# Optimization experiments

Hardware: AMD Instinct MI355X
Metric: run time of the kernel (lower is better)

## Reference

```python
import jax, jax.numpy as jnp
import numpy as np

H = 2048   # hidden_size
NH = 32    # n_head
HS = 64    # head_size
B, T = 2, 4096
D_DECAY, D_AAA, D_MV, D_GATE = 96, 96, 64, 256


def setup_inputs() -> dict:
    key = jax.random.key(0)
    ks = jax.random.split(key, 30)
    rn = lambda k, s, sc=0.02: jax.random.normal(k, s, jnp.float32) * sc
    d = {}
    d['x'] = jax.random.normal(ks[0], (B, T, H), jnp.float32)
    d['shift_state_in'] = jax.random.normal(ks[1], (B, H), jnp.float32)
    d['wkv_state_in'] = jnp.zeros((B, NH, HS, HS), jnp.float32)
    d['v_first_val'] = jax.random.normal(ks[2], (B, T, H), jnp.float32)
    for i, n in enumerate(['x_r', 'x_w', 'x_k', 'x_v', 'x_a', 'x_g']):
        d[n] = jax.random.uniform(ks[3 + i], (H,), jnp.float32)
    d['w0'] = rn(ks[9], (H,)) - 4.0
    d['w1'] = rn(ks[10], (H, D_DECAY)); d['w2'] = rn(ks[11], (D_DECAY, H))
    d['a0'] = rn(ks[12], (H,)); d['a1'] = rn(ks[13], (H, D_AAA)); d['a2'] = rn(ks[14], (D_AAA, H))
    d['v0'] = rn(ks[15], (H,)) + 1.0; d['v1'] = rn(ks[16], (H, D_MV)); d['v2'] = rn(ks[17], (D_MV, H))
    d['g1'] = rn(ks[18], (H, D_GATE)); d['g2'] = rn(ks[19], (D_GATE, H))
    d['k_k'] = jnp.full((H,), 0.85, jnp.float32)
    d['k_a'] = jnp.ones((H,), jnp.float32)
    d['r_k'] = rn(ks[20], (NH, HS))
    s = 1.0 / np.sqrt(H)
    d['W_r'] = jax.random.normal(ks[21], (H, H), jnp.float32) * s
    d['W_k'] = jax.random.normal(ks[22], (H, H), jnp.float32) * s
    d['W_v'] = jax.random.normal(ks[23], (H, H), jnp.float32) * s
    d['W_o'] = jax.random.normal(ks[24], (H, H), jnp.float32) * s
    d['ln_w'] = jnp.ones((H,), jnp.float32)
    d['ln_b'] = jnp.zeros((H,), jnp.float32)
    return d


def _forward(x, shift_state_in, wkv_state_in, v_first_val, x_r, x_w, x_k, x_v, x_a, x_g,
             w0, w1, w2, a0, a1, a2, v0, v1, v2, g1, g2, k_k, k_a, r_k,
             W_r, W_k, W_v, W_o, ln_w, ln_b):
    Bx, Tx, C = x.shape
    # token shift: previous token embedding (shift_state for t=0)
    xprev = jnp.concatenate([shift_state_in[:, None, :], x[:, :-1]], axis=1)
    dx = xprev - x
    xr, xw, xk, xv, xa, xg = (x + dx * m for m in (x_r, x_w, x_k, x_v, x_a, x_g))
    r = xr @ W_r.T
    k = xk @ W_k.T
    v = xv @ W_v.T
    # soft-clamped log-decay (<= -0.5)
    w_raw = -jax.nn.softplus(-(w0 + jnp.tanh(xw @ w1) @ w2)) - 0.5
    # layer_id > 0: residual mix with first-layer value
    v = v + (v_first_val - v) * jax.nn.sigmoid(v0 + (xv @ v1) @ v2)
    a = jax.nn.sigmoid(a0 + (xa @ a1) @ a2)          # in-context learning rate
    g = jax.nn.sigmoid(xg @ g1) @ g2                 # output gate
    kk = (k * k_k).reshape(Bx, Tx, NH, HS)
    kk = kk / jnp.maximum(jnp.linalg.norm(kk, axis=-1, keepdims=True), 1e-12)  # F.normalize
    kk = kk.reshape(Bx, Tx, C)
    k = k * (1.0 + (a - 1.0) * k_a)
    w = jnp.exp(-jnp.exp(w_raw))                     # per-channel decay in (0,1)
    heads = lambda t: t.reshape(Bx, Tx, NH, HS).transpose(1, 0, 2, 3)  # [T,B,NH,HS]
    rs, ws, ks_, vs, kks, as_ = map(heads, (r, w, k, v, kk, a))

    def step(S, inp):
        # S: [B,NH,HS(value),HS(key)]
        rt, wt, kt, vt, kkt, at = inp
        sa = jnp.einsum('bhvk,bhk->bhv', S, -kkt)
        S = (S * wt[:, :, None, :]
             + sa[:, :, :, None] * (kkt * at)[:, :, None, :]
             + vt[:, :, :, None] * kt[:, :, None, :])
        return S, jnp.einsum('bhvk,bhk->bhv', S, rt)

    wkv_state_out, y = jax.lax.scan(step, wkv_state_in, (rs, ws, ks_, vs, kks, as_))
    y = y.transpose(1, 0, 2, 3)                      # [B,T,NH,HS]
    # GroupNorm(n_head groups, eps=1e-5*head_size)
    mu = y.mean(-1, keepdims=True)
    var = y.var(-1, keepdims=True)
    y = ((y - mu) / jnp.sqrt(var + 1e-5 * HS)).reshape(Bx, Tx, C) * ln_w + ln_b
    rk = (r.reshape(Bx, Tx, NH, HS) * k.reshape(Bx, Tx, NH, HS) * r_k).sum(-1, keepdims=True)
    y = y + (rk * v.reshape(Bx, Tx, NH, HS)).reshape(Bx, Tx, C)
    out = (y * g) @ W_o.T
    return out, x[:, -1], wkv_state_out, v_first_val


def reference(x, shift_state_in, wkv_state_in, v_first_val, x_r, x_w, x_k, x_v, x_a, x_g,
              w0, w1, w2, a0, a1, a2, v0, v1, v2, g1, g2, k_k, k_a, r_k,
              W_r, W_k, W_v, W_o, ln_w, ln_b):
    return _forward(x, shift_state_in, wkv_state_in, v_first_val, x_r, x_w, x_k, x_v, x_a, x_g,
                    w0, w1, w2, a0, a1, a2, v0, v1, v2, g1, g2, k_k, k_a, r_k,
                    W_r, W_k, W_v, W_o, ln_w, ln_b)
```

## Files before the change

kernel.cpp:

```cpp
#include <hip/hip_runtime.h>

typedef unsigned short u16;
typedef __attribute__((ext_vector_type(4))) float f32x4;
typedef __attribute__((ext_vector_type(8))) __bf16 bf16x8;
typedef __attribute__((ext_vector_type(8))) unsigned short u16x8;
typedef __attribute__((ext_vector_type(4))) unsigned short u16x4;

#define DI static __device__ __forceinline__

DI float bfu2f(u16 u){ unsigned int x = ((unsigned int)u)<<16; float f; __builtin_memcpy(&f,&x,4); return f; }
DI u16 f2bfu(float f){ __bf16 h = (__bf16)f; u16 u; __builtin_memcpy(&u,&h,2); return u; }
DI float sigm(float x){ return 1.f/(1.f+expf(-x)); }

DI void gload_lds16(const void* g, void* l) {
  __builtin_amdgcn_global_load_lds(
      (const __attribute__((address_space(1))) unsigned int*)g,
      (__attribute__((address_space(3))) unsigned int*)l, 16, 0, 0);
}

template<bool OBF16>
__global__ __launch_bounds__(256) void gemm128_k(
    const u16* __restrict__ A, const u16* __restrict__ Bt,
    void* __restrict__ Cp, int M, int N, int K)
{
  __shared__ alignas(16) u16 As[128*64];
  __shared__ alignas(16) u16 Bs[128*64];
  const int tid = threadIdx.x;
  const int wid = tid >> 6, lane = tid & 63;
  const int wm = wid >> 1, wn = wid & 1;
  const int l15 = lane & 15, q = lane >> 4;
  const int m0 = blockIdx.x * 128, n0 = blockIdx.y * 128;
  const int sr = (wid << 3) + (lane >> 3);
  const int sc = (lane & 7) << 3;
  f32x4 acc[4][4];
  #pragma unroll
  for (int i=0;i<4;i++)
    #pragma unroll
    for (int j=0;j<4;j++) acc[i][j] = f32x4{0.f,0.f,0.f,0.f};

  char* la = (char*)As + (size_t)wid*1024;
  char* lb = (char*)Bs + (size_t)wid*1024;
  for (int k0 = 0; k0 < K; k0 += 64) {
    const u16* ga = A  + (size_t)(m0 + sr)*K + k0 + sc;
    const u16* gb = Bt + (size_t)(n0 + sr)*K + k0 + sc;
    #pragma unroll
    for (int it = 0; it < 4; ++it) {
      gload_lds16(ga + (size_t)(32*it)*K, la + it*4096);
      gload_lds16(gb + (size_t)(32*it)*K, lb + it*4096);
    }
    __syncthreads();
    #pragma unroll
    for (int ks = 0; ks < 64; ks += 32) {
      bf16x8 af[4], bfv[4];
      #pragma unroll
      for (int i=0;i<4;i++) af[i]  = *(const bf16x8*)&As[(wm*64 + i*16 + l15)*64 + ks + q*8];
      #pragma unroll
      for (int j=0;j<4;j++) bfv[j] = *(const bf16x8*)&Bs[(wn*64 + j*16 + l15)*64 + ks + q*8];
      #pragma unroll
      for (int i=0;i<4;i++)
        #pragma unroll
        for (int j=0;j<4;j++)
          acc[i][j] = __builtin_amdgcn_mfma_f32_16x16x32_bf16(af[i], bfv[j], acc[i][j], 0, 0, 0);
    }
    __syncthreads();
  }
  #pragma unroll
  for (int i=0;i<4;i++)
    #pragma unroll
    for (int j=0;j<4;j++)
      #pragma unroll
      for (int rr=0;rr<4;rr++) {
        const int gm = m0 + wm*64 + i*16 + q*4 + rr;
        const int gn = n0 + wn*64 + j*16 + l15;
        const size_t o = (size_t)gm * (size_t)N + gn;
        if constexpr (OBF16) ((u16*)Cp)[o] = f2bfu(acc[i][j][rr]);
        else                 ((float*)Cp)[o] = acc[i][j][rr];
      }
}

constexpr int LDW = 72;

template<bool MIX, bool WNK, bool ABF16, bool OBF16, int EPI=0>
__global__ __launch_bounds__(256) void gemm_k(
    const void* __restrict__ Ap, const float* __restrict__ dxp, const float* __restrict__ mixp,
    const float* __restrict__ Wp, void* __restrict__ Cp, int M, int N, int K)
{
  __shared__ alignas(16) __bf16 As[64*LDW];
  __shared__ alignas(16) __bf16 Bs[64*LDW];
  const int tid = threadIdx.x;
  const int m0 = blockIdx.x * 64;
  const int n0 = blockIdx.y * 64;
  const int lane = tid & 63, wid = tid >> 6;
  const int wm = wid >> 1, wn = wid & 1;
  const int l15 = lane & 15, q = lane >> 4;
  f32x4 acc[2][2] = {{{0.f,0.f,0.f,0.f},{0.f,0.f,0.f,0.f}},
                     {{0.f,0.f,0.f,0.f},{0.f,0.f,0.f,0.f}}};

  for (int k0 = 0; k0 < K; k0 += 64) {
    {
      const int kc = (tid & 7) * 8;
      const int r0 = tid >> 3;
      #pragma unroll
      for (int it = 0; it < 2; ++it) {
        const int row = r0 + 32*it;
        const size_t gmK = (size_t)(m0 + row) * (size_t)K;
        const int gk = k0 + kc;
        if constexpr (ABF16) {
          const u16* A16 = (const u16*)Ap;
          u16x8 u;
          if (gk + 7 < K) u = *(const u16x8*)(A16 + gmK + gk);
          else {
            #pragma unroll
            for (int e=0;e<8;e++) u[e] = (gk+e < K) ? A16[gmK + gk + e] : (u16)0;
          }
          *(u16x8*)&As[row*LDW + kc] = u;
        } else {
          const float* A32 = (const float*)Ap;
          float f[8];
          if (gk + 7 < K) {
            f32x4 va = *(const f32x4*)(A32 + gmK + gk);
            f32x4 vb = *(const f32x4*)(A32 + gmK + gk + 4);
            if constexpr (MIX) {
              f32x4 d0 = *(const f32x4*)(dxp + gmK + gk);
              f32x4 d1 = *(const f32x4*)(dxp + gmK + gk + 4);
              f32x4 c0 = *(const f32x4*)(mixp + gk);
              f32x4 c1 = *(const f32x4*)(mixp + gk + 4);
              va = va + d0*c0; vb = vb + d1*c1;
            }
            #pragma unroll
            for (int e=0;e<4;e++){ f[e]=va[e]; f[4+e]=vb[e]; }
          } else {
            #pragma unroll
            for (int e=0;e<8;e++){
              const int kk2 = gk+e;
              float xv = 0.f;
              if (kk2 < K) {
                xv = A32[gmK + kk2];
                if constexpr (MIX) xv = fmaf(dxp[gmK+kk2], mixp[kk2], xv);
              }
              f[e] = xv;
            }
          }
          bf16x8 v8;
          #pragma unroll
          for (int e=0;e<8;e++) v8[e] = (__bf16)f[e];
          *(bf16x8*)&As[row*LDW + kc] = v8;
        }
      }
    }
    if constexpr (WNK) {
      const int kc = (tid & 7) * 8;
      const int r0 = tid >> 3;
      #pragma unroll
      for (int it = 0; it < 2; ++it) {
        const int row = r0 + 32*it;
        const int gn = n0 + row;
        const int gk = k0 + kc;
        float f[8];
        if (gn < N && gk + 7 < K) {
          const size_t o = (size_t)gn * (size_t)K + gk;
          f32x4 va = *(const f32x4*)(Wp + o);
          f32x4 vb = *(const f32x4*)(Wp + o + 4);
          #pragma unroll
          for (int e=0;e<4;e++){ f[e]=va[e]; f[4+e]=vb[e]; }
        } else {
          #pragma unroll
          for (int e=0;e<8;e++) f[e] = (gn < N && gk+e < K) ? Wp[(size_t)gn*K + gk + e] : 0.f;
        }
        bf16x8 v8;
        #pragma unroll
        for (int e=0;e<8;e++) v8[e] = (__bf16)f[e];
        *(bf16x8*)&Bs[row*LDW + kc] = v8;
      }
    } else {
      const int nc = (tid & 15) * 4;
      const int kr = tid >> 4;
      #pragma unroll
      for (int it = 0; it < 4; ++it) {
        const int kk = kr + 16*it;
        const int gk = k0 + kk;
        f32x4 v = {0.f,0.f,0.f,0.f};
        if (gk < K) {
          const int gn = n0 + nc;
          if (gn + 3 < N) v = *(const f32x4*)(Wp + (size_t)gk*N + gn);
          else {
            #pragma unroll
            for (int e=0;e<4;e++) if (gn+e < N) v[e] = Wp[(size_t)gk*N + gn + e];
          }
        }
        #pragma unroll
        for (int e=0;e<4;e++) Bs[(nc+e)*LDW + kk] = (__bf16)v[e];
      }
    }
    __syncthreads();
    #pragma unroll
    for (int ks = 0; ks < 64; ks += 32) {
      bf16x8 af[2], bfv[2];
      #pragma unroll
      for (int i=0;i<2;i++) af[i]  = *(const bf16x8*)&As[(wm*32 + i*16 + l15)*LDW + ks + q*8];
      #pragma unroll
      for (int i=0;i<2;i++) bfv[i] = *(const bf16x8*)&Bs[(wn*32 + i*16 + l15)*LDW + ks + q*8];
      #pragma unroll
      for (int i=0;i<2;i++)
        #pragma unroll
        for (int j=0;j<2;j++)
          acc[i][j] = __builtin_amdgcn_mfma_f32_16x16x32_bf16(af[i], bfv[j], acc[i][j], 0, 0, 0);
    }
    __syncthreads();
  }
  #pragma unroll
  for (int i=0;i<2;i++) {
    #pragma unroll
    for (int j=0;j<2;j++) {
      #pragma unroll
      for (int rr=0;rr<4;rr++) {
        const int gm = m0 + wm*32 + i*16 + q*4 + rr;
        const int gn = n0 + wn*32 + j*16 + l15;
        if (gn < N) {
          const size_t o = (size_t)gm * (size_t)N + gn;
          const float a = acc[i][j][rr];
          if constexpr (EPI == 1) {
            float* C = (float*)Cp;
            const float s = sigm(mixp[gn] + a);
            const float vG = C[o];
            C[o] = vG + (dxp[o] - vG) * s;
          } else if constexpr (EPI == 2) {
            const float z = -(mixp[gn] + a);
            const float sp = (z > 20.f) ? z : log1pf(expf(z));
            ((float*)Cp)[o] = expf(-expf(-sp - 0.5f));
          } else if constexpr (EPI == 3) {
            ((u16*)Cp)[o] = f2bfu(sigm(mixp[gn] + a));
          } else if constexpr (EPI == 4) {
            ((u16*)Cp)[o] = f2bfu(tanhf(a));
          } else if constexpr (EPI == 5) {
            ((u16*)Cp)[o] = f2bfu(sigm(a));
          } else if constexpr (OBF16) {
            ((u16*)Cp)[o] = f2bfu(a);
          } else {
            ((float*)Cp)[o] = a;
          }
        }
      }
    }
  }
}

__global__ void mix_cast_k(const float* __restrict__ x, const float* __restrict__ shift,
    const float* __restrict__ mr, const float* __restrict__ mw, const float* __restrict__ mk,
    const float* __restrict__ mv, const float* __restrict__ ma, const float* __restrict__ mg,
    u16* __restrict__ xr_b, u16* __restrict__ xw_b, u16* __restrict__ xk_b,
    u16* __restrict__ xv_b, u16* __restrict__ xa_b, u16* __restrict__ xg_b,
    float* __restrict__ xlast, int T_, int B_)
{
  const int Hh = 2048;
  size_t e4 = (size_t)blockIdx.x*blockDim.x + threadIdx.x;
  size_t total4 = (size_t)B_*T_*Hh/4;
  if (e4 >= total4) return;
  size_t e = e4*4;
  size_t th = (size_t)T_*Hh;
  size_t b = e / th; size_t rem = e - b*th;
  int t = (int)(rem / Hh); int c = (int)(rem & (Hh-1));
  f32x4 xv4 = *(const f32x4*)(x+e);
  f32x4 xp = t ? *(const f32x4*)(x+e-Hh) : *(const f32x4*)(shift + b*Hh + c);
  f32x4 dx = xp - xv4;
  if (t == T_-1) *(f32x4*)(xlast + b*Hh + c) = xv4;
  #define EMIT(mp, dst) { \
    f32x4 mc = *(const f32x4*)(mp + c); \
    f32x4 r_ = xv4 + dx*mc; \
    u16x4 o_; \
    o_[0]=f2bfu(r_[0]); o_[1]=f2bfu(r_[1]); o_[2]=f2bfu(r_[2]); o_[3]=f2bfu(r_[3]); \
    *(u16x4*)(dst + e) = o_; }
  EMIT(mr, xr_b) EMIT(mw, xw_b) EMIT(mk, xk_b)
  EMIT(mv, xv_b) EMIT(ma, xa_b) EMIT(mg, xg_b)
  #undef EMIT
}

__global__ void castw_k(const float* __restrict__ src, u16* __restrict__ dst, long n4){
  long i = (long)blockIdx.x*blockDim.x + threadIdx.x;
  if (i < n4) {
    f32x4 v = ((const f32x4*)src)[i];
    u16x4 o; o[0]=f2bfu(v[0]); o[1]=f2bfu(v[1]); o[2]=f2bfu(v[2]); o[3]=f2bfu(v[3]);
    ((u16x4*)dst)[i] = o;
  }
}

__global__ __launch_bounds__(256) void rnorm_k(
    const u16* __restrict__ kb, const float* __restrict__ kkw, float* __restrict__ r2)
{
  const size_t bt = blockIdx.x;
  const int tid = threadIdx.x;
  const int c0 = tid << 3;
  u16x8 kv8 = *(const u16x8*)(kb + bt*2048 + c0);
  f32x4 ka_ = *(const f32x4*)(kkw + c0);
  f32x4 kb_ = *(const f32x4*)(kkw + c0 + 4);
  float s = 0.f;
  #pragma unroll
  for (int e=0;e<4;e++){ float kk = bfu2f(kv8[e])*ka_[e];   s = fmaf(kk,kk,s); }
  #pragma unroll
  for (int e=0;e<4;e++){ float kk = bfu2f(kv8[4+e])*kb_[e]; s = fmaf(kk,kk,s); }
  s += __shfl_xor(s, 1, 64);
  s += __shfl_xor(s, 2, 64);
  s += __shfl_xor(s, 4, 64);
  if ((tid & 7) == 0) r2[bt*32 + (tid>>3)] = 1.f/fmaxf(s, 1e-24f);
}

__global__ __launch_bounds__(64) __attribute__((amdgpu_waves_per_eu(1, 4)))
void scan_k(
    const u16* __restrict__ rb, const float* __restrict__ wb, const u16* __restrict__ kb,
    const float* __restrict__ vb, const u16* __restrict__ ab,
    const float* __restrict__ kkw, const float* __restrict__ kaw,
    const float* __restrict__ S0, float* __restrict__ yb, float* __restrict__ Sout, int T_)
{
  const int Hh = 2048, NHl = 32;
  const int blk = blockIdx.x;
  const int b = blk >> 5, h = blk & 31;
  const int lane = threadIdx.x;
  float S[64];
  const size_t sbase = (((size_t)b*NHl + h)*64 + lane)*64;
  #pragma unroll
  for (int i=0;i<64;i++) S[i] = S0[sbase+i];
  const float kkc = kkw[h*64+lane], kac = kaw[h*64+lane];
  __shared__ alignas(16) float lw[64], lkk[64], lka[64], lke[64], lr[64];
  size_t idx = (size_t)b*T_*Hh + (size_t)h*64 + lane;
  float rv = bfu2f(rb[idx]), wv = wb[idx], kv = bfu2f(kb[idx]), vv = vb[idx], av = bfu2f(ab[idx]);
  for (int t=0; t<T_; ++t) {
    float kk = kv * kkc;
    float ssum = kk*kk;
    #pragma unroll
    for (int m=1;m<64;m<<=1) ssum += __shfl_xor(ssum, m, 64);
    float inv = 1.f / fmaxf(sqrtf(ssum), 1e-12f);
    float kkn = kk * inv;
    float ke  = kv * (1.f + (av - 1.f)*kac);
    lw[lane]=wv; lkk[lane]=kkn; lka[lane]=kkn*av; lke[lane]=ke; lr[lane]=rv;
    const float vt = vv;
    __syncthreads();
    float nrv=0.f,nwv=0.f,nkv=0.f,nvv=0.f,nav=0.f;
    if (t+1 < T_) {
      const size_t ni = idx + Hh;
      nrv = bfu2f(rb[ni]); nwv = wb[ni]; nkv = bfu2f(kb[ni]); nvv = vb[ni]; nav = bfu2f(ab[ni]);
    }
    const f32x4* KK4 = (const f32x4*)lkk;
    const f32x4* W4  = (const f32x4*)lw;
    const f32x4* KA4 = (const f32x4*)lka;
    const f32x4* KE4 = (const f32x4*)lke;
    const f32x4* R4  = (const f32x4*)lr;
    float sa0=0.f,sa1=0.f,sa2=0.f,sa3=0.f;
    #pragma unroll
    for (int qq=0;qq<16;qq++){
      f32x4 k4 = KK4[qq];
      sa0 = fmaf(S[4*qq+0], k4[0], sa0);
      sa1 = fmaf(S[4*qq+1], k4[1], sa1);
      sa2 = fmaf(S[4*qq+2], k4[2], sa2);
      sa3 = fmaf(S[4*qq+3], k4[3], sa3);
    }
    const float sa = -((sa0+sa1)+(sa2+sa3));
    float y0=0.f,y1=0.f,y2=0.f,y3=0.f;
    #pragma unroll
    for (int qq=0;qq<16;qq++){
      f32x4 w4=W4[qq], a4=KA4[qq], e4=KE4[qq], r4=R4[qq];
      float s_;
      s_ = fmaf(vt, e4[0], fmaf(sa, a4[0], S[4*qq+0]*w4[0])); S[4*qq+0]=s_; y0 = fmaf(s_, r4[0], y0);
      s_ = fmaf(vt, e4[1], fmaf(sa, a4[1], S[4*qq+1]*w4[1])); S[4*qq+1]=s_; y1 = fmaf(s_, r4[1], y1);
      s_ = fmaf(vt, e4[2], fmaf(sa, a4[2], S[4*qq+2]*w4[2])); S[4*qq+2]=s_; y2 = fmaf(s_, r4[2], y2);
      s_ = fmaf(vt, e4[3], fmaf(sa, a4[3], S[4*qq+3]*w4[3])); S[4*qq+3]=s_; y3 = fmaf(s_, r4[3], y3);
    }
    yb[idx] = (y0+y1)+(y2+y3);
    __syncthreads();
    rv=nrv; wv=nwv; kv=nkv; vv=nvv; av=nav;
    idx += Hh;
  }
  #pragma unroll
  for (int i=0;i<64;i++) Sout[sbase+i] = S[i];
}

__global__ __launch_bounds__(256) void chunk_mu_k(
    const u16* __restrict__ rb, const float* __restrict__ wb, const u16* __restrict__ kb,
    const float* __restrict__ vb, const u16* __restrict__ ab,
    const float* __restrict__ kkw, const float* __restrict__ kaw,
    const float* __restrict__ r2b,
    float* __restrict__ Mbuf, float* __restrict__ Ubuf, float* __restrict__ Dbuf,
    float* __restrict__ yb, int T_, int NC)
{
  const int wid  = threadIdx.x >> 6;
  const int lane = threadIdx.x & 63;
  const int g    = blockIdx.x * 4 + wid;
  const int ch   = g >> 1;
  const bool mrole = ((g & 1) == 0);
  const int c  = ch % NC;
  const int bh = ch / NC;
  const int b = bh >> 5, h = bh & 31;

  float S[64];
  #pragma unroll
  for (int i=0;i<64;i++) S[i] = (mrole && lane == i) ? 1.f : 0.f;

  const int hc = h*64 + lane;
  const float kkc = kkw[hc], kac = kaw[hc];

  __shared__ alignas(16) float LB[4][3][5][64];
  float (*Lw)[5][64] = LB[wid];

  size_t idx = ((size_t)b*T_ + (size_t)c*64)*2048 + hc;
  size_t r2i = ((size_t)b*T_ + (size_t)c*64)*32 + h;
  float* dD = Dbuf + (size_t)ch*4096 + lane;

  {
    const float kv = bfu2f(kb[idx]);
    const float av = bfu2f(ab[idx]);
    const float kk = kv*kkc;
    Lw[0][0][lane] = wb[idx];
    Lw[0][1][lane] = kk;
    Lw[0][2][lane] = kk*av;
    Lw[0][3][lane] = kv*(1.f+(av-1.f)*kac);
    Lw[0][4][lane] = bfu2f(rb[idx]);
  }
  float c_vv = mrole ? 0.f : vb[idx];
  float c_r2 = r2b[r2i];
  float p_r, p_k, p_w, p_a, p_v = 0.f, p_r2;
  {
    const size_t ni = idx + 2048;
    p_r = bfu2f(rb[ni]); p_k = bfu2f(kb[ni]); p_w = wb[ni]; p_a = bfu2f(ab[ni]);
    if (!mrole) p_v = vb[ni];
    p_r2 = r2b[r2i + 32];
  }

  int cur = 0;
  for (int j=0; j<64; ++j) {
    int nxt = cur + 1; if (nxt == 3) nxt = 0;
    if (j+1 < 64) {
      const float kk = p_k*kkc;
      Lw[nxt][0][lane] = p_w;
      Lw[nxt][1][lane] = kk;
      Lw[nxt][2][lane] = kk*p_a;
      Lw[nxt][3][lane] = p_k*(1.f+(p_a-1.f)*kac);
      Lw[nxt][4][lane] = p_r;
    }
    const float n_vv = p_v, n_r2 = p_r2;
    float q_r=0.f,q_k=0.f,q_w=0.f,q_a=0.f,q_v=0.f,q_r2=0.f;
    if (j+2 < 64) {
      const size_t ni = idx + 4096;
      q_r = bfu2f(rb[ni]); q_k = bfu2f(kb[ni]); q_w = wb[ni]; q_a = bfu2f(ab[ni]);
      if (!mrole) q_v = vb[ni];
      q_r2 = r2b[r2i + 64];
    }
    const f32x4* W4  = (const f32x4*)Lw[cur][0];
    const f32x4* KK4 = (const f32x4*)Lw[cur][1];
    const f32x4* KA4 = (const f32x4*)Lw[cur][2];
    const f32x4* KE4 = (const f32x4*)Lw[cur][3];
    const f32x4* R4  = (const f32x4*)Lw[cur][4];
    float sA0=0.f,sA1=0.f,sA2=0.f,sA3=0.f,sB0=0.f,sB1=0.f,sB2=0.f,sB3=0.f;
    #pragma unroll
    for (int qq=0;qq<8;qq++){
      f32x4 kA = KK4[qq];
      sA0 = fmaf(S[4*qq+0], kA[0], sA0);
      sA1 = fmaf(S[4*qq+1], kA[1], sA1);
      sA2 = fmaf(S[4*qq+2], kA[2], sA2);
      sA3 = fmaf(S[4*qq+3], kA[3], sA3);
      f32x4 kB = KK4[8+qq];
      sB0 = fmaf(S[32+4*qq+0], kB[0], sB0);
      sB1 = fmaf(S[32+4*qq+1], kB[1], sB1);
      sB2 = fmaf(S[32+4*qq+2], kB[2], sB2);
      sB3 = fmaf(S[32+4*qq+3], kB[3], sB3);
    }
    const float sa = -(((sA0+sB0)+(sA1+sB1)) + ((sA2+sB2)+(sA3+sB3))) * c_r2;
    const float vt = c_vv;
    float y0=0.f,y1=0.f,y2=0.f,y3=0.f;
    if (mrole) {
      #pragma unroll
      for (int qq=0;qq<16;qq++){
        f32x4 w4=W4[qq], a4=KA4[qq], r4=R4[qq];
        float s_;
        s_ = fmaf(sa, a4[0], S[4*qq+0]*w4[0]); S[4*qq+0]=s_; y0 = fmaf(s_, r4[0], y0);
        s_ = fmaf(sa, a4[1], S[4*qq+1]*w4[1]); S[4*qq+1]=s_; y1 = fmaf(s_, r4[1], y1);
        s_ = fmaf(sa, a4[2], S[4*qq+2]*w4[2]); S[4*qq+2]=s_; y2 = fmaf(s_, r4[2], y2);
        s_ = fmaf(sa, a4[3], S[4*qq+3]*w4[3]); S[4*qq+3]=s_; y3 = fmaf(s_, r4[3], y3);
      }
      dD[(size_t)j*64] = (y0+y1)+(y2+y3);
    } else {
      #pragma unroll
      for (int qq=0;qq<16;qq++){
        f32x4 w4=W4[qq], a4=KA4[qq], e4=KE4[qq], r4=R4[qq];
        float s_;
        s_ = fmaf(vt, e4[0], fmaf(sa, a4[0], S[4*qq+0]*w4[0])); S[4*qq+0]=s_; y0 = fmaf(s_, r4[0], y0);
        s_ = fmaf(vt, e4[1], fmaf(sa, a4[1], S[4*qq+1]*w4[1])); S[4*qq+1]=s_; y1 = fmaf(s_, r4[1], y1);
        s_ = fmaf(vt, e4[2], fmaf(sa, a4[2], S[4*qq+2]*w4[2])); S[4*qq+2]=s_; y2 = fmaf(s_, r4[2], y2);
        s_ = fmaf(vt, e4[3], fmaf(sa, a4[3], S[4*qq+3]*w4[3])); S[4*qq+3]=s_; y3 = fmaf(s_, r4[3], y3);
      }
      yb[idx] = (y0+y1)+(y2+y3);
    }
    cur = nxt;
    c_vv = n_vv; c_r2 = n_r2;
    p_r=q_r; p_k=q_k; p_w=q_w; p_a=q_a; p_v=q_v; p_r2=q_r2;
    idx += 2048; r2i += 32;
  }
  float* fd = (mrole ? Mbuf : Ubuf) + (size_t)ch*4096 + (size_t)lane*64;
  #pragma unroll
  for (int qq=0;qq<16;qq++)
    *(f32x4*)(fd + 4*qq) = f32x4{S[4*qq+0],S[4*qq+1],S[4*qq+2],S[4*qq+3]};
}

__global__ __launch_bounds__(256) void propagate_k(
    const float* __restrict__ Mbuf, const float* Ubuf,
    const float* __restrict__ S0, float* SSbuf, float* __restrict__ Sout, int NC)
{
  const int bh   = blockIdx.x >> 2;
  const int v0r  = (blockIdx.x & 3) * 16;
  const int tid  = threadIdx.x;
  const int lane = tid & 63;
  const int wvv  = tid >> 6;

  __shared__ float MT[64*65];
  __shared__ float Srow[16][64];

  #pragma unroll
  for (int i=0;i<4;i++) {
    const int v = v0r + wvv*4 + i;
    Srow[wvv*4+i][lane] = S0[((size_t)bh*64 + v)*64 + lane];
  }

  const size_t mbase = (size_t)bh * NC * 4096;
  f32x4 mreg[4];
  #pragma unroll
  for (int it=0; it<4; ++it)
    mreg[it] = *(const f32x4*)(Mbuf + mbase + it*1024 + tid*4);

  for (int c=0; c<NC; ++c) {
    const size_t chB = mbase + (size_t)c*4096;
    #pragma unroll
    for (int it=0; it<4; ++it) {
      const int base = it*1024 + tid*4;
      const int j = base >> 6;
      const int k = base & 63;
      #pragma unroll
      for (int e=0;e<4;e++) MT[(k+e)*65 + j] = mreg[it][e];
    }
    __syncthreads();
    if (c+1 < NC) {
      #pragma unroll
      for (int it=0; it<4; ++it)
        mreg[it] = *(const f32x4*)(Mbuf + chB + 4096 + it*1024 + tid*4);
    }
    float u[4];
    #pragma unroll
    for (int i=0;i<4;i++)
      u[i] = Ubuf[chB + (size_t)(v0r + wvv*4 + i)*64 + lane];
    #pragma unroll
    for (int i=0;i<4;i++)
      SSbuf[chB + (size_t)(v0r + wvv*4 + i)*64 + lane] = Srow[wvv*4+i][lane];
    float acc[4] = {0.f,0.f,0.f,0.f};
    #pragma unroll
    for (int j4=0; j4<16; ++j4) {
      float m0_ = MT[lane*65 + j4*4 + 0];
      float m1_ = MT[lane*65 + j4*4 + 1];
      float m2_ = MT[lane*65 + j4*4 + 2];
      float m3_ = MT[lane*65 + j4*4 + 3];
      #pragma unroll
      for (int i=0;i<4;i++) {
        f32x4 s4 = *(const f32x4*)&Srow[wvv*4+i][j4*4];
        acc[i] = fmaf(s4[0], m0_, acc[i]);
        acc[i] = fmaf(s4[1], m1_, acc[i]);
        acc[i] = fmaf(s4[2], m2_, acc[i]);
        acc[i] = fmaf(s4[3], m3_, acc[i]);
      }
    }
    #pragma unroll
    for (int i=0;i<4;i++) Srow[wvv*4+i][lane] = acc[i] + u[i];
    __syncthreads();
  }
  #pragma unroll
  for (int i=0;i<4;i++) {
    const int v = v0r + wvv*4 + i;
    Sout[((size_t)bh*64 + v)*64 + lane] = Srow[wvv*4+i][lane];
  }
}

__global__ __launch_bounds__(256) void ycorr_k(
    const float* __restrict__ SSbuf, const float* __restrict__ Dbuf,
    float* __restrict__ yb, int T_, int NC)
{
  const int ch = blockIdx.x;
  const int c  = ch % NC;
  const int bh = ch / NC;
  const int b = bh >> 5, h = bh & 31;
  const int tid = threadIdx.x;
  const int wid = tid >> 6, lane = tid & 63;

  __shared__ alignas(16) float Sl[64*68];
  __shared__ alignas(16) float Dl[64*68];

  {
    const float* sg = SSbuf + (size_t)ch*4096;
    const float* dg = Dbuf  + (size_t)ch*4096;
    #pragma unroll
    for (int i=0;i<4;i++){
      const int o = i*1024 + tid*4;
      f32x4 vs = *(const f32x4*)(sg + o);
      f32x4 vd = *(const f32x4*)(dg + o);
      const int rr = o >> 6, cc = o & 63;
      *(f32x4*)&Sl[rr*68 + cc] = vs;
      *(f32x4*)&Dl[rr*68 + cc] = vd;
    }
  }
  __syncthreads();
  float ss[64];
  #pragma unroll
  for (int qq=0;qq<16;qq++){
    f32x4 v = *(const f32x4*)&Sl[lane*68 + 4*qq];
    ss[4*qq+0]=v[0]; ss[4*qq+1]=v[1]; ss[4*qq+2]=v[2]; ss[4*qq+3]=v[3];
  }
  size_t idx = ((size_t)b*T_ + (size_t)c*64 + (size_t)wid*16)*2048 + (size_t)h*64 + lane;
  for (int tt=0; tt<16; ++tt) {
    const f32x4* D4 = (const f32x4*)&Dl[(wid*16 + tt)*68];
    float a0=0.f,a1=0.f,a2=0.f,a3=0.f;
    #pragma unroll
    for (int qq=0;qq<16;qq++){
      f32x4 d4 = D4[qq];
      a0 = fmaf(ss[4*qq+0], d4[0], a0);
      a1 = fmaf(ss[4*qq+1], d4[1], a1);
      a2 = fmaf(ss[4*qq+2], d4[2], a2);
      a3 = fmaf(ss[4*qq+3], d4[3], a3);
    }
    yb[idx] = yb[idx] + ((a0+a1)+(a2+a3));
    idx += 2048;
  }
}

__global__ __launch_bounds__(256) void post_k(
    const float* __restrict__ yb, const u16* __restrict__ rb, const u16* __restrict__ kb,
    const u16* __restrict__ ab, const u16* __restrict__ gb, const float* vb,
    const float* __restrict__ kaw, const float* __restrict__ rkw,
    const float* __restrict__ lnw, const float* __restrict__ lnb, u16* __restrict__ zb,
    const float* __restrict__ vf, float* vout)
{
  const int wid = threadIdx.x >> 6, lane = threadIdx.x & 63;
  const size_t unit = (size_t)blockIdx.x*4 + wid;
  const size_t bt = unit >> 5; const int h = (int)(unit & 31);
  const size_t idx = bt*2048 + (size_t)h*64 + lane;
  const int hc = h*64 + lane;
  const float yv = yb[idx];
  const float rv = bfu2f(rb[idx]), kv = bfu2f(kb[idx]), av = bfu2f(ab[idx]);
  const float vbv = vb[idx];
  const float ke = kv*(1.f + (av-1.f)*kaw[hc]);
  float s1 = yv, s2 = yv*yv, rk = rv*ke*rkw[hc];
  #pragma unroll
  for (int m=1;m<64;m<<=1){
    s1 += __shfl_xor(s1,m,64);
    s2 += __shfl_xor(s2,m,64);
    rk += __shfl_xor(rk,m,64);
  }
  const float mean = s1 * (1.f/64.f);
  const float var  = s2 * (1.f/64.f) - mean*mean;
  const float rstd = rsqrtf(var + 6.4e-4f);
  const float zn = (yv-mean)*rstd*lnw[hc] + lnb[hc] + rk*vbv;
  zb[idx] = f2bfu(zn * bfu2f(gb[idx]));
  vout[idx] = vf[idx];
}

extern "C" void kernel_launch(void* const* d_in, const int* in_sizes, int n_in,
                              void* d_out, int out_size, void* d_ws, size_t ws_size,
                              hipStream_t stream)
{
  const float* x      = (const float*)d_in[0];
  const float* shift  = (const float*)d_in[1];
  const float* wkv0   = (const float*)d_in[2];
  const float* vfirst = (const float*)d_in[3];
  const float* xr = (const float*)d_in[4];
  const float* xw = (const float*)d_in[5];
  const float* xk = (const float*)d_in[6];
  const float* xv = (const float*)d_in[7];
  const float* xa = (const float*)d_in[8];
  const float* xg = (const float*)d_in[9];
  const float* w0 = (const float*)d_in[10];
  const float* w1 = (const float*)d_in[11];
  const float* w2 = (const float*)d_in[12];
  const float* a0 = (const float*)d_in[13];
  const float* a1 = (const float*)d_in[14];
  const float* a2 = (const float*)d_in[15];
  const float* v0 = (const float*)d_in[16];
  const float* v1 = (const float*)d_in[17];
  const float* v2 = (const float*)d_in[18];
  const float* g1 = (const float*)d_in[19];
  const float* g2 = (const float*)d_in[20];
  const float* k_k = (const float*)d_in[21];
  const float* k_a = (const float*)d_in[22];
  const float* r_k = (const float*)d_in[23];
  const float* W_r = (const float*)d_in[24];
  const float* W_k = (const float*)d_in[25];
  const float* W_v = (const float*)d_in[26];
  const float* W_o = (const float*)d_in[27];
  const float* ln_w = (const float*)d_in[28];
  const float* ln_b = (const float*)d_in[29];

  const int H = 2048, NH = 32;
  const int BH = in_sizes[1];
  const int B  = BH / H;
  const long BTH = (long)in_sizes[0];
  const int T  = (int)(BTH / BH);
  const int M  = (int)(BTH / H);

  float* out0 = (float*)d_out;
  float* out1 = out0 + BTH;
  float* out2 = out1 + BH;
  float* out3 = out2 + (size_t)B*NH*64*64;

  char* ws = (char*)d_ws;
  u16* mixb = (u16*)ws;  ws += (size_t)BTH*12;
  u16* xr_b = mixb + 0*BTH;
  u16* xw_b = mixb + 1*BTH;
  u16* xk_b = mixb + 2*BTH;
  u16* xv_b = mixb + 3*BTH;
  u16* xa_b = mixb + 4*BTH;
  u16* xg_b = mixb + 5*BTH;
  float* Mbuf  = (float*)mixb;
  float* Ubuf  = Mbuf + BTH;
  float* Dbuf  = Ubuf + BTH;
  float* SSbuf = Ubuf;
  u16*   zb16  = (u16*)mixb;
  u16* rb   = (u16*)ws;  ws += BTH*2;
  u16* kb   = (u16*)ws;  ws += BTH*2;
  u16* ab   = (u16*)ws;  ws += BTH*2;
  u16* gb   = (u16*)ws;  ws += BTH*2;
  u16* wr16 = (u16*)ws;  ws += (size_t)H*H*2;
  u16* wk16 = (u16*)ws;  ws += (size_t)H*H*2;
  u16* wv16 = (u16*)ws;  ws += (size_t)H*H*2;
  u16* wo16 = (u16*)ws;  ws += (size_t)H*H*2;
  u16* h1w  = (u16*)ws;  ws += (size_t)M*96*2;
  u16* h1a  = (u16*)ws;  ws += (size_t)M*96*2;
  u16* h1v  = (u16*)ws;  ws += (size_t)M*64*2;
  u16* h1g  = (u16*)ws;  ws += (size_t)M*256*2;
  float* dxz = (float*)ws; ws += BTH*4;
  float* r2b = (float*)h1w;
  const size_t ws_need = (size_t)(ws - (char*)d_ws);
  const bool chunked = (ws_size >= ws_need) && (T % 64 == 0);
  const bool big_ok  = (M % 128 == 0);
  (void)n_in; (void)out_size;

  const dim3 blk(256);
  auto gg  = [&](int N){ return dim3(M/64, (N+63)/64); };
  auto gg128 = [&](int N){ return dim3(M/128, N/128); };

  mix_cast_k<<<dim3((unsigned)((BTH/4 + 255)/256)), blk, 0, stream>>>(
      x, shift, xr, xw, xk, xv, xa, xg, xr_b, xw_b, xk_b, xv_b, xa_b, xg_b, out1, T, B);

  {
    const long n4 = (long)H*H/4;
    const dim3 gw((unsigned)((n4 + 255)/256));
    castw_k<<<gw, blk, 0, stream>>>(W_r, wr16, n4);
    castw_k<<<gw, blk, 0, stream>>>(W_k, wk16, n4);
    castw_k<<<gw, blk, 0, stream>>>(W_v, wv16, n4);
    castw_k<<<gw, blk, 0, stream>>>(W_o, wo16, n4);
  }

  gemm_k<false,false,true,true,4><<<gg(96),  blk, 0, stream>>>(xw_b, nullptr, nullptr, w1, h1w, M, 96,  H);
  gemm_k<false,false,true,true  ><<<gg(96),  blk, 0, stream>>>(xa_b, nullptr, nullptr, a1, h1a, M, 96,  H);
  gemm_k<false,false,true,true  ><<<gg(64),  blk, 0, stream>>>(xv_b, nullptr, nullptr, v1, h1v, M, 64,  H);
  gemm_k<false,false,true,true,5><<<gg(256), blk, 0, stream>>>(xg_b, nullptr, nullptr, g1, h1g, M, 256, H);

  if (big_ok) {
    gemm128_k<true ><<<gg128(H), blk, 0, stream>>>(xr_b, wr16, rb,   M, H, H);
    gemm128_k<true ><<<gg128(H), blk, 0, stream>>>(xk_b, wk16, kb,   M, H, H);
    gemm128_k<false><<<gg128(H), blk, 0, stream>>>(xv_b, wv16, out3, M, H, H);
  } else {
    gemm_k<false,true,true,true ><<<gg(H), blk, 0, stream>>>(xr_b, nullptr, nullptr, W_r, rb,   M, H, H);
    gemm_k<false,true,true,true ><<<gg(H), blk, 0, stream>>>(xk_b, nullptr, nullptr, W_k, kb,   M, H, H);
    gemm_k<false,true,true,false><<<gg(H), blk, 0, stream>>>(xv_b, nullptr, nullptr, W_v, out3, M, H, H);
  }

  gemm_k<false,false,true,false,2><<<gg(H), blk, 0, stream>>>(h1w, nullptr, w0, w2, dxz, M, H, 96);
  rnorm_k<<<dim3((unsigned)M), blk, 0, stream>>>(kb, k_k, r2b);
  gemm_k<false,false,true,true,3 ><<<gg(H), blk, 0, stream>>>(h1a, nullptr, a0, a2, ab,  M, H, 96);
  gemm_k<false,false,true,false,1><<<gg(H), blk, 0, stream>>>(h1v, vfirst,  v0, v2, out3, M, H, 64);
  gemm_k<false,false,true,true   ><<<gg(H), blk, 0, stream>>>(h1g, nullptr, nullptr, g2, gb,  M, H, 256);

  if (chunked) {
    const int NC = T / 64;
    const int CH = B * NH * NC;
    chunk_mu_k <<<dim3((unsigned)(2*CH/4)), blk, 0, stream>>>(rb, dxz, kb, out3, ab, k_k, k_a, r2b,
                                                              Mbuf, Ubuf, Dbuf, out0, T, NC);
    propagate_k<<<dim3(B*NH*4), blk, 0, stream>>>(Mbuf, Ubuf, wkv0, SSbuf, out2, NC);
    ycorr_k    <<<dim3(CH),     blk, 0, stream>>>(SSbuf, Dbuf, out0, T, NC);
  } else {
    scan_k<<<dim3(B*NH), dim3(64), 0, stream>>>(rb, dxz, kb, out3, ab, k_k, k_a, wkv0, out0, out2, T);
  }

  post_k<<<dim3((unsigned)((size_t)M*NH/4)), blk, 0, stream>>>(out0, rb, kb, ab, gb, out3,
                                                               k_a, r_k, ln_w, ln_b, zb16,
                                                               vfirst, out3);

  if (big_ok) {
    gemm128_k<false><<<gg128(H), blk, 0, stream>>>(zb16, wo16, out0, M, H, H);
  } else {
    gemm_k<false,true,true,false><<<gg(H), blk, 0, stream>>>(zb16, nullptr, nullptr, W_o, out0, M, H, H);
  }
}
```

Before: 1.849 ms.

## Merge M and U chunk roles into one wave and batch weight casts

The chunk kernel now has one wave compute both the M (transition) state and the U (value-driven) state for a chunk, where before these were split across two waves. The per-step LDS staging and the global loads of r/k/w/a/v are now shared between the two states, and the LDS ring shrinks from triple to double buffering. Each wave now keeps 128 state registers, which raises register pressure and halves the number of waves. Separately, the four weight-cast launches are merged into one launch over a 2D grid.

Measured after the change: 2.046 ms. 1.11x slower.

```diff
diff --git a/kernel.cpp b/kernel.cpp
--- a/kernel.cpp
+++ b/kernel.cpp
@@ -275,13 +275,19 @@
   #undef EMIT
 }
 
-__global__ void castw_k(const float* __restrict__ src, u16* __restrict__ dst, long n4){
+__global__ void castw4_k(
+    const float* __restrict__ s0, const float* __restrict__ s1,
+    const float* __restrict__ s2, const float* __restrict__ s3,
+    u16* __restrict__ d0, u16* __restrict__ d1,
+    u16* __restrict__ d2, u16* __restrict__ d3, long n4)
+{
   long i = (long)blockIdx.x*blockDim.x + threadIdx.x;
-  if (i < n4) {
-    f32x4 v = ((const f32x4*)src)[i];
-    u16x4 o; o[0]=f2bfu(v[0]); o[1]=f2bfu(v[1]); o[2]=f2bfu(v[2]); o[3]=f2bfu(v[3]);
-    ((u16x4*)dst)[i] = o;
-  }
+  if (i >= n4) return;
+  const float* src = (blockIdx.y == 0) ? s0 : (blockIdx.y == 1) ? s1 : (blockIdx.y == 2) ? s2 : s3;
+  u16* dst = (blockIdx.y == 0) ? d0 : (blockIdx.y == 1) ? d1 : (blockIdx.y == 2) ? d2 : d3;
+  f32x4 v = ((const f32x4*)src)[i];
+  u16x4 o; o[0]=f2bfu(v[0]); o[1]=f2bfu(v[1]); o[2]=f2bfu(v[2]); o[3]=f2bfu(v[3]);
+  ((u16x4*)dst)[i] = o;
 }
 
 __global__ __launch_bounds__(256) void rnorm_k(
@@ -383,21 +389,19 @@
 {
   const int wid  = threadIdx.x >> 6;
   const int lane = threadIdx.x & 63;
-  const int g    = blockIdx.x * 4 + wid;
-  const int ch   = g >> 1;
-  const bool mrole = ((g & 1) == 0);
+  const int ch   = blockIdx.x * 4 + wid;
   const int c  = ch % NC;
   const int bh = ch / NC;
   const int b = bh >> 5, h = bh & 31;
 
-  float S[64];
-  #pragma unroll
-  for (int i=0;i<64;i++) S[i] = (mrole && lane == i) ? 1.f : 0.f;
+  float SM[64], SU[64];
+  #pragma unroll
+  for (int i=0;i<64;i++) { SM[i] = (lane == i) ? 1.f : 0.f; SU[i] = 0.f; }
 
   const int hc = h*64 + lane;
   const float kkc = kkw[hc], kac = kaw[hc];
 
-  __shared__ alignas(16) float LB[4][3][5][64];
+  __shared__ alignas(16) float LB[4][2][5][64];
   float (*Lw)[5][64] = LB[wid];
 
   size_t idx = ((size_t)b*T_ + (size_t)c*64)*2048 + hc;
@@ -414,89 +418,82 @@
     Lw[0][3][lane] = kv*(1.f+(av-1.f)*kac);
     Lw[0][4][lane] = bfu2f(rb[idx]);
   }
-  float c_vv = mrole ? 0.f : vb[idx];
+  float c_vv = vb[idx];
   float c_r2 = r2b[r2i];
-  float p_r, p_k, p_w, p_a, p_v = 0.f, p_r2;
+  float p_r=0.f, p_k=0.f, p_w=0.f, p_a=0.f, p_v=0.f, p_r2=0.f;
   {
     const size_t ni = idx + 2048;
     p_r = bfu2f(rb[ni]); p_k = bfu2f(kb[ni]); p_w = wb[ni]; p_a = bfu2f(ab[ni]);
-    if (!mrole) p_v = vb[ni];
+    p_v = vb[ni];
     p_r2 = r2b[r2i + 32];
   }
 
-  int cur = 0;
   for (int j=0; j<64; ++j) {
-    int nxt = cur + 1; if (nxt == 3) nxt = 0;
+    const int cur = j & 1;
     if (j+1 < 64) {
       const float kk = p_k*kkc;
-      Lw[nxt][0][lane] = p_w;
-      Lw[nxt][1][lane] = kk;
-      Lw[nxt][2][lane] = kk*p_a;
-      Lw[nxt][3][lane] = p_k*(1.f+(p_a-1.f)*kac);
-      Lw[nxt][4][lane] = p_r;
+      Lw[cur^1][0][lane] = p_w;
+      Lw[cur^1][1][lane] = kk;
+      Lw[cur^1][2][lane] = kk*p_a;
+      Lw[cur^1][3][lane] = p_k*(1.f+(p_a-1.f)*kac);
+      Lw[cur^1][4][lane] = p_r;
     }
     const float n_vv = p_v, n_r2 = p_r2;
-    float q_r=0.f,q_k=0.f,q_w=0.f,q_a=0.f,q_v=0.f,q_r2=0.f;
     if (j+2 < 64) {
       const size_t ni = idx + 4096;
-      q_r = bfu2f(rb[ni]); q_k = bfu2f(kb[ni]); q_w = wb[ni]; q_a = bfu2f(ab[ni]);
-      if (!mrole) q_v = vb[ni];
-      q_r2 = r2b[r2i + 64];
+      p_r = bfu2f(rb[ni]); p_k = bfu2f(kb[ni]); p_w = wb[ni]; p_a = bfu2f(ab[ni]);
+      p_v = vb[ni];
+      p_r2 = r2b[r2i + 64];
     }
     const f32x4* W4  = (const f32x4*)Lw[cur][0];
     const f32x4* KK4 = (const f32x4*)Lw[cur][1];
     const f32x4* KA4 = (const f32x4*)Lw[cur][2];
     const f32x4* KE4 = (const f32x4*)Lw[cur][3];
     const f32x4* R4  = (const f32x4*)Lw[cur][4];
-    float sA0=0.f,sA1=0.f,sA2=0.f,sA3=0.f,sB0=0.f,sB1=0.f,sB2=0.f,sB3=0.f;
-    #pragma unroll
-    for (int qq=0;qq<8;qq++){
-      f32x4 kA = KK4[qq];
-      sA0 = fmaf(S[4*qq+0], kA[0], sA0);
-      sA1 = fmaf(S[4*qq+1], kA[1], sA1);
-      sA2 = fmaf(S[4*qq+2], kA[2], sA2);
-      sA3 = fmaf(S[4*qq+3], kA[3], sA3);
-      f32x4 kB = KK4[8+qq];
-      sB0 = fmaf(S[32+4*qq+0], kB[0], sB0);
-      sB1 = fmaf(S[32+4*qq+1], kB[1], sB1);
-      sB2 = fmaf(S[32+4*qq+2], kB[2], sB2);
-      sB3 = fmaf(S[32+4*qq+3], kB[3], sB3);
-    }
-    const float sa = -(((sA0+sB0)+(sA1+sB1)) + ((sA2+sB2)+(sA3+sB3))) * c_r2;
+    float m0=0.f,m1=0.f,m2=0.f,m3=0.f;
+    float u0=0.f,u1=0.f,u2=0.f,u3=0.f;
+    #pragma unroll
+    for (int qq=0;qq<16;qq++){
+      f32x4 k4 = KK4[qq];
+      m0 = fmaf(SM[4*qq+0], k4[0], m0);
+      m1 = fmaf(SM[4*qq+1], k4[1], m1);
+      m2 = fmaf(SM[4*qq+2], k4[2], m2);
+      m3 = fmaf(SM[4*qq+3], k4[3], m3);
+      u0 = fmaf(SU[4*qq+0], k4[0], u0);
+      u1 = fmaf(SU[4*qq+1], k4[1], u1);
+      u2 = fmaf(SU[4*qq+2], k4[2], u2);
+      u3 = fmaf(SU[4*qq+3], k4[3], u3);
+    }
+    const float saM = -((m0+m1)+(m2+m3)) * c_r2;
+    const float saU = -((u0+u1)+(u2+u3)) * c_r2;
     const float vt = c_vv;
+    float d0=0.f,d1=0.f,d2=0.f,d3=0.f;
     float y0=0.f,y1=0.f,y2=0.f,y3=0.f;
-    if (mrole) {
-      #pragma unroll
-      for (int qq=0;qq<16;qq++){
-        f32x4 w4=W4[qq], a4=KA4[qq], r4=R4[qq];
-        float s_;
-        s_ = fmaf(sa, a4[0], S[4*qq+0]*w4[0]); S[4*qq+0]=s_; y0 = fmaf(s_, r4[0], y0);
-        s_ = fmaf(sa, a4[1], S[4*qq+1]*w4[1]); S[4*qq+1]=s_; y1 = fmaf(s_, r4[1], y1);
-        s_ = fmaf(sa, a4[2], S[4*qq+2]*w4[2]); S[4*qq+2]=s_; y2 = fmaf(s_, r4[2], y2);
-        s_ = fmaf(sa, a4[3], S[4*qq+3]*w4[3]); S[4*qq+3]=s_; y3 = fmaf(s_, r4[3], y3);
-      }
-      dD[(size_t)j*64] = (y0+y1)+(y2+y3);
-    } else {
-      #pragma unroll
-      for (int qq=0;qq<16;qq++){
-        f32x4 w4=W4[qq], a4=KA4[qq], e4=KE4[qq], r4=R4[qq];
-        float s_;
-        s_ = fmaf(vt, e4[0], fmaf(sa, a4[0], S[4*qq+0]*w4[0])); S[4*qq+0]=s_; y0 = fmaf(s_, r4[0], y0);
-        s_ = fmaf(vt, e4[1], fmaf(sa, a4[1], S[4*qq+1]*w4[1])); S[4*qq+1]=s_; y1 = fmaf(s_, r4[1], y1);
-        s_ = fmaf(vt, e4[2], fmaf(sa, a4[2], S[4*qq+2]*w4[2])); S[4*qq+2]=s_; y2 = fmaf(s_, r4[2], y2);
-        s_ = fmaf(vt, e4[3], fmaf(sa, a4[3], S[4*qq+3]*w4[3])); S[4*qq+3]=s_; y3 = fmaf(s_, r4[3], y3);
-      }
-      yb[idx] = (y0+y1)+(y2+y3);
-    }
-    cur = nxt;
+    #pragma unroll
+    for (int qq=0;qq<16;qq++){
+      f32x4 w4=W4[qq], a4=KA4[qq], e4=KE4[qq], r4=R4[qq];
+      float s_;
+      s_ = fmaf(saM, a4[0], SM[4*qq+0]*w4[0]); SM[4*qq+0]=s_; d0 = fmaf(s_, r4[0], d0);
+      s_ = fmaf(saM, a4[1], SM[4*qq+1]*w4[1]); SM[4*qq+1]=s_; d1 = fmaf(s_, r4[1], d1);
+      s_ = fmaf(saM, a4[2], SM[4*qq+2]*w4[2]); SM[4*qq+2]=s_; d2 = fmaf(s_, r4[2], d2);
+      s_ = fmaf(saM, a4[3], SM[4*qq+3]*w4[3]); SM[4*qq+3]=s_; d3 = fmaf(s_, r4[3], d3);
+      s_ = fmaf(vt, e4[0], fmaf(saU, a4[0], SU[4*qq+0]*w4[0])); SU[4*qq+0]=s_; y0 = fmaf(s_, r4[0], y0);
+      s_ = fmaf(vt, e4[1], fmaf(saU, a4[1], SU[4*qq+1]*w4[1])); SU[4*qq+1]=s_; y1 = fmaf(s_, r4[1], y1);
+      s_ = fmaf(vt, e4[2], fmaf(saU, a4[2], SU[4*qq+2]*w4[2])); SU[4*qq+2]=s_; y2 = fmaf(s_, r4[2], y2);
+      s_ = fmaf(vt, e4[3], fmaf(saU, a4[3], SU[4*qq+3]*w4[3])); SU[4*qq+3]=s_; y3 = fmaf(s_, r4[3], y3);
+    }
+    dD[(size_t)j*64] = (d0+d1)+(d2+d3);
+    yb[idx] = (y0+y1)+(y2+y3);
     c_vv = n_vv; c_r2 = n_r2;
-    p_r=q_r; p_k=q_k; p_w=q_w; p_a=q_a; p_v=q_v; p_r2=q_r2;
     idx += 2048; r2i += 32;
   }
-  float* fd = (mrole ? Mbuf : Ubuf) + (size_t)ch*4096 + (size_t)lane*64;
-  #pragma unroll
-  for (int qq=0;qq<16;qq++)
-    *(f32x4*)(fd + 4*qq) = f32x4{S[4*qq+0],S[4*qq+1],S[4*qq+2],S[4*qq+3]};
+  float* md = Mbuf + (size_t)ch*4096 + (size_t)lane*64;
+  float* ud = Ubuf + (size_t)ch*4096 + (size_t)lane*64;
+  #pragma unroll
+  for (int qq=0;qq<16;qq++){
+    *(f32x4*)(md + 4*qq) = f32x4{SM[4*qq+0],SM[4*qq+1],SM[4*qq+2],SM[4*qq+3]};
+    *(f32x4*)(ud + 4*qq) = f32x4{SU[4*qq+0],SU[4*qq+1],SU[4*qq+2],SU[4*qq+3]};
+  }
 }
 
 __global__ __launch_bounds__(256) void propagate_k(
@@ -744,11 +741,8 @@
 
   {
     const long n4 = (long)H*H/4;
-    const dim3 gw((unsigned)((n4 + 255)/256));
-    castw_k<<<gw, blk, 0, stream>>>(W_r, wr16, n4);
-    castw_k<<<gw, blk, 0, stream>>>(W_k, wk16, n4);
-    castw_k<<<gw, blk, 0, stream>>>(W_v, wv16, n4);
-    castw_k<<<gw, blk, 0, stream>>>(W_o, wo16, n4);
+    castw4_k<<<dim3((unsigned)((n4 + 255)/256), 4), blk, 0, stream>>>(
+        W_r, W_k, W_v, W_o, wr16, wk16, wv16, wo16, n4);
   }
 
   gemm_k<false,false,true,true,4><<<gg(96),  blk, 0, stream>>>(xw_b, nullptr, nullptr, w1, h1w, M, 96,  H);
@@ -775,8 +769,8 @@
   if (chunked) {
     const int NC = T / 64;
     const int CH = B * NH * NC;
-    chunk_mu_k <<<dim3((unsigned)(2*CH/4)), blk, 0, stream>>>(rb, dxz, kb, out3, ab, k_k, k_a, r2b,
-                                                              Mbuf, Ubuf, Dbuf, out0, T, NC);
+    chunk_mu_k <<<dim3((unsigned)(CH/4)), blk, 0, stream>>>(rb, dxz, kb, out3, ab, k_k, k_a, r2b,
+                                                            Mbuf, Ubuf, Dbuf, out0, T, NC);
     propagate_k<<<dim3(B*NH*4), blk, 0, stream>>>(Mbuf, Ubuf, wkv0, SSbuf, out2, NC);
     ycorr_k    <<<dim3(CH),     blk, 0, stream>>>(SSbuf, Dbuf, out0, T, NC);
   } else {
```

## Add 256x256 double-buffered MFMA GEMM for large projections and fuse weight casts

Applied to the files above, without the earlier changes.

Adds a 512-thread GEMM kernel with 256x256 output tiles, double-buffered LDS staging via global_load_lds, prefetch of the next K tile overlapped with MFMA work, and setprio around the MFMA bursts. It replaces the 128x128 kernel for the four HxH projections when M is divisible by 256, raising data reuse per block and aiming to hide load latency. The four weight-cast launches are also merged into one 2D-grid launch to cut launch overhead. The large tile uses 128 KB of LDS and 128 accumulator floats per thread. With M=8192 and N=2048 that gives only 256 blocks, which may leave occupancy low and the wave count uneven across CUs.

Result: slower. 1.898 ms (+2.7%).

```diff
diff --git a/kernel.cpp b/kernel.cpp
--- a/kernel.cpp
+++ b/kernel.cpp
@@ -16,6 +16,101 @@
   __builtin_amdgcn_global_load_lds(
       (const __attribute__((address_space(1))) unsigned int*)g,
       (__attribute__((address_space(3))) unsigned int*)l, 16, 0, 0);
+}
+
+template<bool OBF16>
+__global__ __launch_bounds__(512) void gemm256_k(
+    const u16* __restrict__ A, const u16* __restrict__ Bt,
+    void* __restrict__ Cp, int M, int N, int K)
+{
+  __shared__ alignas(16) u16 As[2][2][128*64];
+  __shared__ alignas(16) u16 Bs[2][2][128*64];
+  const int tid = threadIdx.x;
+  const int wid = tid >> 6, lane = tid & 63;
+  const int wm = wid >> 2, wn = wid & 3;
+  const int l15 = lane & 15, ql = lane >> 4;
+  const int m0 = blockIdx.x * 256, n0 = blockIdx.y * 256;
+  const int NT = K >> 6;
+
+  f32x4 acc[8][4];
+  #pragma unroll
+  for (int i=0;i<8;i++)
+    #pragma unroll
+    for (int j=0;j<4;j++) acc[i][j] = f32x4{0.f,0.f,0.f,0.f};
+
+  const int sgrow = 8*wid + (lane>>3);
+  const int sgcol = (lane&7) << 3;
+  const int slo   = wid*512;
+
+  auto stageTile = [&](int kt){
+    const int buf = kt & 1;
+    const int k0 = kt << 6;
+    #pragma unroll
+    for (int h=0; h<2; ++h)
+      #pragma unroll
+      for (int r=0; r<2; ++r){
+        const int lo = r*4096 + slo;
+        const int grow = h*128 + 64*r + sgrow;
+        gload_lds16(A  + (size_t)(m0 + grow)*K + k0 + sgcol, (char*)&As[buf][h][lo]);
+        gload_lds16(Bt + (size_t)(n0 + grow)*K + k0 + sgcol, (char*)&Bs[buf][h][lo]);
+      }
+  };
+
+  stageTile(0);
+  asm volatile("s_waitcnt vmcnt(0)" ::: "memory");
+  __builtin_amdgcn_sched_barrier(0);
+  __builtin_amdgcn_s_barrier();
+  __builtin_amdgcn_sched_barrier(0);
+
+  for (int kt=0; kt<NT; ++kt){
+    const int buf = kt & 1;
+    #pragma unroll
+    for (int q=0; q<4; ++q){
+      const int mh = q>>1, nh = q&1;
+      bf16x8 af[4][2], bfv[2][2];
+      #pragma unroll
+      for (int i=0;i<4;i++)
+        #pragma unroll
+        for (int ks=0;ks<2;ks++)
+          af[i][ks] = *(const bf16x8*)&As[buf][wm][((mh*4+i)*16 + l15)*64 + ks*32 + ql*8];
+      #pragma unroll
+      for (int j=0;j<2;j++)
+        #pragma unroll
+        for (int ks=0;ks<2;ks++)
+          bfv[j][ks] = *(const bf16x8*)&Bs[buf][wn>>1][((wn&1)*64 + (nh*2+j)*16 + l15)*64 + ks*32 + ql*8];
+      if (q==0 && kt+1 < NT) stageTile(kt+1);
+      __builtin_amdgcn_sched_barrier(0);
+      __builtin_amdgcn_s_barrier();
+      __builtin_amdgcn_sched_barrier(0);
+      __builtin_amdgcn_s_setprio(1);
+      #pragma unroll
+      for (int i=0;i<4;i++)
+        #pragma unroll
+        for (int j=0;j<2;j++)
+          #pragma unroll
+          for (int ks=0;ks<2;ks++)
+            acc[mh*4+i][nh*2+j] = __builtin_amdgcn_mfma_f32_16x16x32_bf16(
+                af[i][ks], bfv[j][ks], acc[mh*4+i][nh*2+j], 0, 0, 0);
+      __builtin_amdgcn_s_setprio(0);
+      if (q==3) { asm volatile("s_waitcnt vmcnt(0)" ::: "memory"); }
+      __builtin_amdgcn_sched_barrier(0);
+      __builtin_amdgcn_s_barrier();
+      __builtin_amdgcn_sched_barrier(0);
+    }
+  }
+
+  #pragma unroll
+  for (int i=0;i<8;i++)
+    #pragma unroll
+    for (int j=0;j<4;j++)
+      #pragma unroll
+      for (int rr=0;rr<4;rr++) {
+        const int gm = m0 + wm*128 + i*16 + ql*4 + rr;
+        const int gn = n0 + wn*64 + j*16 + l15;
+        const size_t o = (size_t)gm * (size_t)N + gn;
+        if constexpr (OBF16) ((u16*)Cp)[o] = f2bfu(acc[i][j][rr]);
+        else                 ((float*)Cp)[o] = acc[i][j][rr];
+      }
 }
 
 template<bool OBF16>
@@ -275,13 +370,19 @@
   #undef EMIT
 }
 
-__global__ void castw_k(const float* __restrict__ src, u16* __restrict__ dst, long n4){
+__global__ void castw4_k(
+    const float* __restrict__ s0, const float* __restrict__ s1,
+    const float* __restrict__ s2, const float* __restrict__ s3,
+    u16* __restrict__ d0, u16* __restrict__ d1,
+    u16* __restrict__ d2, u16* __restrict__ d3, long n4)
+{
   long i = (long)blockIdx.x*blockDim.x + threadIdx.x;
-  if (i < n4) {
-    f32x4 v = ((const f32x4*)src)[i];
-    u16x4 o; o[0]=f2bfu(v[0]); o[1]=f2bfu(v[1]); o[2]=f2bfu(v[2]); o[3]=f2bfu(v[3]);
-    ((u16x4*)dst)[i] = o;
-  }
+  if (i >= n4) return;
+  const float* src = (blockIdx.y == 0) ? s0 : (blockIdx.y == 1) ? s1 : (blockIdx.y == 2) ? s2 : s3;
+  u16* dst = (blockIdx.y == 0) ? d0 : (blockIdx.y == 1) ? d1 : (blockIdx.y == 2) ? d2 : d3;
+  f32x4 v = ((const f32x4*)src)[i];
+  u16x4 o; o[0]=f2bfu(v[0]); o[1]=f2bfu(v[1]); o[2]=f2bfu(v[2]); o[3]=f2bfu(v[3]);
+  ((u16x4*)dst)[i] = o;
 }
 
 __global__ __launch_bounds__(256) void rnorm_k(
@@ -732,23 +833,22 @@
   float* r2b = (float*)h1w;
   const size_t ws_need = (size_t)(ws - (char*)d_ws);
   const bool chunked = (ws_size >= ws_need) && (T % 64 == 0);
-  const bool big_ok  = (M % 128 == 0);
+  const bool big256_ok = (M % 256 == 0);
+  const bool big_ok    = (M % 128 == 0);
   (void)n_in; (void)out_size;
 
   const dim3 blk(256);
   auto gg  = [&](int N){ return dim3(M/64, (N+63)/64); };
   auto gg128 = [&](int N){ return dim3(M/128, N/128); };
+  auto gg256 = [&](int N){ return dim3(M/256, N/256); };
 
   mix_cast_k<<<dim3((unsigned)((BTH/4 + 255)/256)), blk, 0, stream>>>(
       x, shift, xr, xw, xk, xv, xa, xg, xr_b, xw_b, xk_b, xv_b, xa_b, xg_b, out1, T, B);
 
   {
     const long n4 = (long)H*H/4;
-    const dim3 gw((unsigned)((n4 + 255)/256));
-    castw_k<<<gw, blk, 0, stream>>>(W_r, wr16, n4);
-    castw_k<<<gw, blk, 0, stream>>>(W_k, wk16, n4);
-    castw_k<<<gw, blk, 0, stream>>>(W_v, wv16, n4);
-    castw_k<<<gw, blk, 0, stream>>>(W_o, wo16, n4);
+    castw4_k<<<dim3((unsigned)((n4 + 255)/256), 4), blk, 0, stream>>>(
+        W_r, W_k, W_v, W_o, wr16, wk16, wv16, wo16, n4);
   }
 
   gemm_k<false,false,true,true,4><<<gg(96),  blk, 0, stream>>>(xw_b, nullptr, nullptr, w1, h1w, M, 96,  H);
@@ -756,7 +856,11 @@
   gemm_k<false,false,true,true  ><<<gg(64),  blk, 0, stream>>>(xv_b, nullptr, nullptr, v1, h1v, M, 64,  H);
   gemm_k<false,false,true,true,5><<<gg(256), blk, 0, stream>>>(xg_b, nullptr, nullptr, g1, h1g, M, 256, H);
 
-  if (big_ok) {
+  if (big256_ok) {
+    gemm256_k<true ><<<gg256(H), dim3(512), 0, stream>>>(xr_b, wr16, rb,   M, H, H);
+    gemm256_k<true ><<<gg256(H), dim3(512), 0, stream>>>(xk_b, wk16, kb,   M, H, H);
+    gemm256_k<false><<<gg256(H), dim3(512), 0, stream>>>(xv_b, wv16, out3, M, H, H);
+  } else if (big_ok) {
     gemm128_k<true ><<<gg128(H), blk, 0, stream>>>(xr_b, wr16, rb,   M, H, H);
     gemm128_k<true ><<<gg128(H), blk, 0, stream>>>(xk_b, wk16, kb,   M, H, H);
     gemm128_k<false><<<gg128(H), blk, 0, stream>>>(xv_b, wv16, out3, M, H, H);
@@ -787,7 +891,9 @@
                                                                k_a, r_k, ln_w, ln_b, zb16,
                                                                vfirst, out3);
 
-  if (big_ok) {
+  if (big256_ok) {
+    gemm256_k<false><<<gg256(H), dim3(512), 0, stream>>>(zb16, wo16, out0, M, H, H);
+  } else if (big_ok) {
     gemm128_k<false><<<gg128(H), blk, 0, stream>>>(zb16, wo16, out0, M, H, H);
   } else {
     gemm_k<false,true,true,false><<<gg(H), blk, 0, stream>>>(zb16, nullptr, nullptr, W_o, out0, M, H, H);
```
